# Kernel tuning notes

Measured on AMD Instinct MI355X. Metric: run time of the kernel, lower is better.

The kernel has to match this reference:

```python
import jax, jax.numpy as jnp
import numpy as np

D_MODEL = 2048
N_HEADS = 16
D_HEAD = D_MODEL // N_HEADS
ROPE_THETA = 10000.0


def setup_inputs() -> dict:
    key = jax.random.key(0)
    ks = jax.random.split(key, 3)
    B, T = 4, 2048
    x = jax.random.normal(ks[0], (B, T, D_MODEL), dtype=jnp.float32)
    # torch Linear weights stored transposed to (in, out) so y = x @ w + b
    w_qkv = jax.random.normal(ks[1], (D_MODEL, 3 * D_MODEL), dtype=jnp.float32) * (1.0 / np.sqrt(D_MODEL))
    b_qkv = jnp.zeros((3 * D_MODEL,), dtype=jnp.float32)
    w_out = jax.random.normal(ks[2], (D_MODEL, D_MODEL), dtype=jnp.float32) * (1.0 / np.sqrt(D_MODEL))
    b_out = jnp.zeros((D_MODEL,), dtype=jnp.float32)
    return {"x": x, "w_qkv": w_qkv, "b_qkv": b_qkv, "w_out": w_out, "b_out": b_out}


def _apply_rope(t, position_offset=0):
    # t: (B, H, T, d_head). Standard rotate-half RoPE.
    T = t.shape[2]
    inv_freq = 1.0 / (ROPE_THETA ** (jnp.arange(0, D_HEAD, 2, dtype=jnp.float32) / D_HEAD))
    pos = jnp.arange(T, dtype=jnp.float32) + position_offset
    freqs = jnp.einsum("t,f->tf", pos, inv_freq)            # (T, d_head/2)
    emb = jnp.concatenate([freqs, freqs], axis=-1)           # (T, d_head)
    cos = jnp.cos(emb)[None, None, :, :]
    sin = jnp.sin(emb)[None, None, :, :]
    t1, t2 = jnp.split(t, 2, axis=-1)
    rot = jnp.concatenate([-t2, t1], axis=-1)
    return t * cos + rot * sin


def reference(x, w_qkv, b_qkv, w_out, b_out):
    B, T, D = x.shape
    scale = 1.0 / np.sqrt(D_HEAD)
    qkv = x @ w_qkv + b_qkv                                   # (B, T, 3D)
    q, k, v = jnp.split(qkv, 3, axis=-1)
    def to_heads(a):
        return a.reshape(B, T, N_HEADS, D_HEAD).transpose(0, 2, 1, 3)  # (B,H,T,dh)
    q, k, v = to_heads(q), to_heads(k), to_heads(v)
    q = _apply_rope(q)
    k = _apply_rope(k)
    scores = jnp.einsum("bhqd,bhkd->bhqk", q, k) * scale      # (B,H,T,T)
    causal = jnp.triu(jnp.full((T, T), -jnp.inf, dtype=scores.dtype), k=1)
    scores = scores + causal
    attn = jax.nn.softmax(scores, axis=-1)                    # dropout p=0 (eval)
    ctx = jnp.einsum("bhqk,bhkd->bhqd", attn, v)
    ctx = ctx.transpose(0, 2, 1, 3).reshape(B, T, D)
    out = ctx @ w_out + b_out
    return out
```

## Files before the change

kernel.cpp:

```cpp
#include <hip/hip_runtime.h>

#define D_MODEL 2048
#define NHEADS 16
#define DHEAD 128
#define TSEQ 2048
#define BATCH 4
#define MROWS (BATCH*TSEQ)
#define NQKV (3*D_MODEL)
#define BH (BATCH*NHEADS)

typedef __attribute__((ext_vector_type(4))) float f32x4;
typedef __attribute__((ext_vector_type(8))) __bf16 bf16x8;
typedef __attribute__((ext_vector_type(4))) unsigned int u32x4;

__device__ inline unsigned short f2bf(float f) {
  union { float f; unsigned u; } v; v.f = f;
  unsigned r = (v.u + 0x7fffu + ((v.u >> 16) & 1u)) >> 16;
  return (unsigned short)r;
}
__device__ inline float bf2f(unsigned short h) {
  union { unsigned u; float f; } v; v.u = ((unsigned)h) << 16; return v.f;
}

__device__ inline void gl_lds16(const unsigned short* g, unsigned short* l) {
  __builtin_amdgcn_global_load_lds(
      (const __attribute__((address_space(1))) unsigned int*)g,
      (__attribute__((address_space(3))) unsigned int*)l, 16, 0, 0);
}

#define CFENCE asm volatile("" ::: "memory")
#define BAR do { CFENCE; __builtin_amdgcn_s_barrier(); CFENCE; } while (0)
#define VM(n) asm volatile("s_waitcnt vmcnt(" #n ")" ::: "memory")
#define LGKM0 asm volatile("s_waitcnt lgkmcnt(0)" ::: "memory")

__global__ __launch_bounds__(256) void cvt_bf16(const float* __restrict__ in,
                                                unsigned short* __restrict__ out, int n) {
  int i = (blockIdx.x * 256 + threadIdx.x) * 8;
  if (i >= n) return;
  float4 a = *(const float4*)(in + i);
  float4 b = *(const float4*)(in + i + 4);
  union { unsigned short s[8]; u32x4 v; } r;
  r.s[0] = f2bf(a.x); r.s[1] = f2bf(a.y); r.s[2] = f2bf(a.z); r.s[3] = f2bf(a.w);
  r.s[4] = f2bf(b.x); r.s[5] = f2bf(b.y); r.s[6] = f2bf(b.z); r.s[7] = f2bf(b.w);
  *(u32x4*)(out + i) = r.v;
}

__global__ __launch_bounds__(256) void transw(const float* __restrict__ w,
                                              unsigned short* __restrict__ wt, int K, int N) {
  __shared__ float tile[32][33];
  int n0 = blockIdx.x * 32, k0 = blockIdx.y * 32;
  int x = threadIdx.x & 31, y = threadIdx.x >> 5;
  #pragma unroll
  for (int j = 0; j < 4; ++j)
    tile[y + j * 8][x] = w[(size_t)(k0 + y + j * 8) * N + n0 + x];
  __syncthreads();
  #pragma unroll
  for (int j = 0; j < 4; ++j)
    wt[(size_t)(n0 + y + j * 8) * K + k0 + x] = f2bf(tile[x][y + j * 8]);
}

__global__ void rope_table(float2* __restrict__ tab) {
  int t = blockIdx.x, f = threadIdx.x;
  float inv = __expf(-0.14391156831212787f * (float)f);
  float ang = (float)t * inv;
  tab[t * 64 + f] = make_float2(cosf(ang), sinf(ang));
}

__global__ __launch_bounds__(256) void rope_apply(unsigned short* __restrict__ X,
                                                  const float2* __restrict__ tab,
                                                  float osc) {
  int row = blockIdx.x * 4 + (threadIdx.x >> 6);
  int f = threadIdx.x & 63;
  int t = row & (TSEQ - 1);
  unsigned short* p = X + (size_t)row * DHEAD;
  float2 cs = tab[t * 64 + f];
  float x1 = bf2f(p[f]), x2 = bf2f(p[f + 64]);
  p[f]      = f2bf((x1 * cs.x - x2 * cs.y) * osc);
  p[f + 64] = f2bf((x2 * cs.x + x1 * cs.y) * osc);
}

template<int MH, int NH>
__device__ inline void mmaq(f32x4 (&acc)[8][4], const bf16x8 (&av)[4][2], const bf16x8 (&bv)[2][2]) {
  #pragma unroll
  for (int m = 0; m < 4; ++m)
    #pragma unroll
    for (int n = 0; n < 2; ++n)
      #pragma unroll
      for (int kk = 0; kk < 2; ++kk)
        acc[MH * 4 + m][NH * 2 + n] =
            __builtin_amdgcn_mfma_f32_16x16x32_bf16(av[m][kk], bv[n][kk],
                                                    acc[MH * 4 + m][NH * 2 + n], 0, 0, 0);
}

__device__ inline void rdhalf(bf16x8 (&dst)[4][2], const unsigned short* base,
                              int rbase, int l15, int l16) {
  #pragma unroll
  for (int m = 0; m < 4; ++m)
    #pragma unroll
    for (int kk = 0; kk < 2; ++kk)
      dst[m][kk] = *(const bf16x8*)&base[(rbase + m * 16 + l15) * 64 +
                                         ((((kk << 2) | l16) ^ (l15 & 7)) << 3)];
}

__device__ inline void rdhalf2(bf16x8 (&dst)[2][2], const unsigned short* base,
                               int rbase, int l15, int l16) {
  #pragma unroll
  for (int n = 0; n < 2; ++n)
    #pragma unroll
    for (int kk = 0; kk < 2; ++kk)
      dst[n][kk] = *(const bf16x8*)&base[(rbase + n * 16 + l15) * 64 +
                                         ((((kk << 2) | l16) ^ (l15 & 7)) << 3)];
}

template<int MODE>
__global__ __launch_bounds__(512, 2) void gemm_bt(
    const unsigned short* __restrict__ A,
    const unsigned short* __restrict__ Bt,
    const float* __restrict__ bias,
    int M, int N, int K,
    unsigned short* __restrict__ Qb,
    unsigned short* __restrict__ Kb,
    unsigned short* __restrict__ VTb,
    float* __restrict__ outF)
{
  __shared__ unsigned short A_lds[2][2][128 * 64];
  __shared__ unsigned short B_lds[2][2][128 * 64];
  int tid = threadIdx.x;
  int wid = tid >> 6, lane = tid & 63;
  int wm = wid >> 2, wn = wid & 3;
  int l15 = lane & 15, l16 = lane >> 4;
  int row0 = blockIdx.y * 256, col0 = blockIdx.x * 256;

  const unsigned short* Ab = A + (size_t)row0 * K;
  const unsigned short* Bb = Bt + (size_t)col0 * K;
  int r8 = tid >> 3;
  int koff = (((tid & 7) ^ (r8 & 7)) << 3);

#define STAGE_A(par, h, tc) do { \
    const unsigned short* g_ = Ab + (size_t)((h) * 128 + r8) * K + (tc) + koff; \
    gl_lds16(g_, &A_lds[par][h][tid * 8]); \
    gl_lds16(g_ + (size_t)64 * K, &A_lds[par][h][(512 + tid) * 8]); } while (0)
#define STAGE_B(par, h, tc) do { \
    const unsigned short* g_ = Bb + (size_t)((h) * 128 + r8) * K + (tc) + koff; \
    gl_lds16(g_, &B_lds[par][h][tid * 8]); \
    gl_lds16(g_ + (size_t)64 * K, &B_lds[par][h][(512 + tid) * 8]); } while (0)

  f32x4 acc[8][4] = {};
  bf16x8 a0[4][2], a1[4][2], b0[2][2], b1[2][2];
  int NT = K >> 6;

  STAGE_A(0, 0, 0); STAGE_B(0, 0, 0); STAGE_A(0, 1, 0); STAGE_B(0, 1, 0);
  VM(4); BAR;

  for (int kt = 0; kt < NT - 1; ++kt) {
    int par = kt & 1, parn = par ^ 1;
    int kn = (kt + 1) << 6;
    rdhalf(a0, &A_lds[par][0][0], wm * 64, l15, l16);
    rdhalf2(b0, &B_lds[par][0][0], wn * 32, l15, l16);
    STAGE_A(parn, 0, kn); STAGE_B(parn, 0, kn);
    VM(6); BAR; LGKM0;
    __builtin_amdgcn_s_setprio(1);
    mmaq<0, 0>(acc, a0, b0);
    __builtin_amdgcn_s_setprio(0);
    rdhalf(a1, &A_lds[par][1][0], wm * 64, l15, l16);
    STAGE_A(parn, 1, kn);
    VM(6); BAR; LGKM0;
    __builtin_amdgcn_s_setprio(1);
    mmaq<1, 0>(acc, a1, b0);
    __builtin_amdgcn_s_setprio(0);
    rdhalf2(b1, &B_lds[par][1][0], wn * 32, l15, l16);
    STAGE_B(parn, 1, kn);
    __builtin_amdgcn_s_setprio(1);
    mmaq<0, 1>(acc, a0, b1);
    __builtin_amdgcn_s_setprio(0);
    VM(4); BAR;
    __builtin_amdgcn_s_setprio(1);
    mmaq<1, 1>(acc, a1, b1);
    __builtin_amdgcn_s_setprio(0);
  }

  {
    int par = (NT - 1) & 1;
    rdhalf(a0, &A_lds[par][0][0], wm * 64, l15, l16);
    rdhalf2(b0, &B_lds[par][0][0], wn * 32, l15, l16);
    VM(2); BAR; LGKM0;
    __builtin_amdgcn_s_setprio(1);
    mmaq<0, 0>(acc, a0, b0);
    __builtin_amdgcn_s_setprio(0);
    rdhalf(a1, &A_lds[par][1][0], wm * 64, l15, l16);
    VM(0); BAR;
    rdhalf2(b1, &B_lds[par][1][0], wn * 32, l15, l16);
    __builtin_amdgcn_s_setprio(1);
    mmaq<1, 0>(acc, a1, b0);
    mmaq<0, 1>(acc, a0, b1);
    mmaq<1, 1>(acc, a1, b1);
    __builtin_amdgcn_s_setprio(0);
  }

  #pragma unroll
  for (int am = 0; am < 8; ++am) {
    int mh = am >> 2, m = am & 3;
    #pragma unroll
    for (int an = 0; an < 4; ++an) {
      int nh = an >> 1, n = an & 1;
      int col = col0 + nh * 128 + wn * 32 + n * 16 + l15;
      float bs = bias[col];
      #pragma unroll
      for (int r = 0; r < 4; ++r) {
        int row = row0 + mh * 128 + wm * 64 + m * 16 + l16 * 4 + r;
        float val = acc[am][an][r] + bs;
        if (MODE == 0) {
          int which = col >> 11;
          int rem = col & 2047;
          int h = rem >> 7, dh = rem & 127;
          int b = row >> 11, t = row & 2047;
          int bh = b * NHEADS + h;
          if (which == 0)      Qb[((size_t)bh * TSEQ + t) * DHEAD + dh] = f2bf(val);
          else if (which == 1) Kb[((size_t)bh * TSEQ + t) * DHEAD + dh] = f2bf(val);
          else                 VTb[((size_t)bh * DHEAD + dh) * TSEQ + t] = f2bf(val);
        } else {
          outF[(size_t)row * N + col] = val;
        }
      }
    }
  }
#undef STAGE_A
#undef STAGE_B
}

__global__ __launch_bounds__(256, 2) void attn_fwd(
    const unsigned short* __restrict__ Qb,
    const unsigned short* __restrict__ Kb,
    const unsigned short* __restrict__ VTb,
    unsigned short* __restrict__ ctx)
{
  __shared__ unsigned short Ksm[2][64 * 128];
  __shared__ unsigned short Vsm[2][128 * 64];
  __shared__ unsigned short Psm[4][32 * 64];
  int bid = blockIdx.x;
  int bh = bid & 63, pr = bid >> 6;
  int hi = 15 - pr, lo = pr;
  int tid = threadIdx.x, wid = tid >> 6, lane = tid & 63;
  int l15 = lane & 15, l16 = lane >> 4;
  const unsigned short* Kh = Kb + (size_t)bh * TSEQ * DHEAD;
  const unsigned short* Vh = VTb + (size_t)bh * DHEAD * TSEQ;
  unsigned short* P = &Psm[wid][0];
  int swzl = (l15 & 7) << 4;

  int krow = tid >> 4;
  int kcol = (((tid & 15) << 4) ^ ((krow & 7) << 4)) >> 1;
  int vrow = tid >> 3;
  int vcol = (((tid & 7) << 4) ^ ((vrow & 7) << 4)) >> 1;
  int ldsl = tid * 8;

  int ck[4];
  #pragma unroll
  for (int kk = 0; kk < 4; ++kk) ck[kk] = ((kk * 64 + l16 * 16) ^ swzl) >> 1;

  bf16x8 qf[2][4];
  f32x4 accO[2][8];
  float mrow[2][4], lrow[2][4];

  int qbase = hi * 128 + wid * 32;
  #pragma unroll
  for (int m = 0; m < 2; ++m) {
    #pragma unroll
    for (int n = 0; n < 8; ++n) accO[m][n] = (f32x4)0.f;
    #pragma unroll
    for (int r = 0; r < 4; ++r) { mrow[m][r] = -1e30f; lrow[m][r] = 0.f; }
    #pragma unroll
    for (int kk = 0; kk < 4; ++kk)
      qf[m][kk] = *(const bf16x8*)&Qb[((size_t)bh * TSEQ + qbase + m * 16 + l15) * DHEAD
                                      + kk * 32 + l16 * 8];
  }

  int nt0 = 2 * hi + 2;
  int ntt = nt0 + 2 * lo + 2;

  {
    const unsigned short* kg = Kh + krow * DHEAD + kcol;
    const unsigned short* vg = Vh + (size_t)vrow * TSEQ + vcol;
    #pragma unroll
    for (int ps = 0; ps < 4; ++ps) {
      gl_lds16(kg + ps * 16 * DHEAD, &Ksm[0][ldsl + ps * 2048]);
      gl_lds16(vg + (size_t)ps * 32 * TSEQ, &Vsm[0][ldsl + ps * 2048]);
    }
  }
  __syncthreads();

  for (int it = 0; it < ntt; ++it) {
    int buf = it & 1;
    int kv0 = ((it >= nt0) ? (it - nt0) : it) * 64;

    if (it + 1 < ntt) {
      int n2 = it + 1;
      int kv2 = ((n2 >= nt0) ? (n2 - nt0) : n2) * 64;
      const unsigned short* kg = Kh + (size_t)(kv2 + krow) * DHEAD + kcol;
      const unsigned short* vg = Vh + (size_t)vrow * TSEQ + kv2 + vcol;
      #pragma unroll
      for (int ps = 0; ps < 4; ++ps) {
        gl_lds16(kg + ps * 16 * DHEAD, &Ksm[buf ^ 1][ldsl + ps * 2048]);
        gl_lds16(vg + (size_t)ps * 32 * TSEQ, &Vsm[buf ^ 1][ldsl + ps * 2048]);
      }
    }

    if (kv0 <= qbase + 31) {
      const unsigned short* Kt = Ksm[buf];
      const unsigned short* Vt = Vsm[buf];

      f32x4 S[2][4] = {};
      #pragma unroll
      for (int n = 0; n < 4; ++n) {
        bf16x8 kf[4];
        #pragma unroll
        for (int kk = 0; kk < 4; ++kk)
          kf[kk] = *(const bf16x8*)&Kt[(n * 16 + l15) * DHEAD + ck[kk]];
        #pragma unroll
        for (int m = 0; m < 2; ++m)
          #pragma unroll
          for (int kk = 0; kk < 4; ++kk)
            S[m][n] = __builtin_amdgcn_mfma_f32_16x16x32_bf16(qf[m][kk], kf[kk], S[m][n], 0, 0, 0);
      }

      bool masked = (kv0 + 63 > qbase);
      float vm_[2][4];
      float grow = -1e30f;
      #pragma unroll
      for (int m = 0; m < 2; ++m) {
        #pragma unroll
        for (int r = 0; r < 4; ++r) {
          if (masked) {
            int qg = qbase + m * 16 + l16 * 4 + r;
            if (kv0 + l15      > qg) S[m][0][r] = -1e30f;
            if (kv0 + 16 + l15 > qg) S[m][1][r] = -1e30f;
            if (kv0 + 32 + l15 > qg) S[m][2][r] = -1e30f;
            if (kv0 + 48 + l15 > qg) S[m][3][r] = -1e30f;
          }
          float v = fmaxf(fmaxf(S[m][0][r], S[m][1][r]), fmaxf(S[m][2][r], S[m][3][r]));
          #pragma unroll
          for (int off = 1; off < 16; off <<= 1) v = fmaxf(v, __shfl_xor(v, off));
          vm_[m][r] = v;
          grow = fmaxf(grow, v - mrow[m][r]);
        }
      }

      if (__any(grow > 8.f)) {
        #pragma unroll
        for (int m = 0; m < 2; ++m)
          #pragma unroll
          for (int r = 0; r < 4; ++r) {
            float mnew = fmaxf(mrow[m][r], vm_[m][r]);
            float alpha = exp2f(mrow[m][r] - mnew);
            mrow[m][r] = mnew;
            lrow[m][r] *= alpha;
            #pragma unroll
            for (int n = 0; n < 8; ++n) accO[m][n][r] *= alpha;
          }
      }

      #pragma unroll
      for (int m = 0; m < 2; ++m) {
        #pragma unroll
        for (int r = 0; r < 4; ++r) {
          float mr = mrow[m][r];
          float p0 = exp2f(S[m][0][r] - mr), p1 = exp2f(S[m][1][r] - mr);
          float p2 = exp2f(S[m][2][r] - mr), p3 = exp2f(S[m][3][r] - mr);
          float ps = (p0 + p1) + (p2 + p3);
          #pragma unroll
          for (int off = 1; off < 16; off <<= 1) ps += __shfl_xor(ps, off);
          lrow[m][r] += ps;
          int qr = m * 16 + l16 * 4 + r;
          int ws = (qr & 7) << 4;
          P[qr * 64 + ((((l15 << 1))      ^ ws) >> 1)] = f2bf(p0);
          P[qr * 64 + (((32 + (l15 << 1)) ^ ws) >> 1)] = f2bf(p1);
          P[qr * 64 + (((64 + (l15 << 1)) ^ ws) >> 1)] = f2bf(p2);
          P[qr * 64 + (((96 + (l15 << 1)) ^ ws) >> 1)] = f2bf(p3);
        }
      }

      bf16x8 pf[2][2];
      #pragma unroll
      for (int m = 0; m < 2; ++m)
        #pragma unroll
        for (int kk = 0; kk < 2; ++kk)
          pf[m][kk] = *(const bf16x8*)&P[(m * 16 + l15) * 64 + ck[kk]];
      #pragma unroll
      for (int n = 0; n < 8; ++n) {
        bf16x8 vf[2];
        #pragma unroll
        for (int kk = 0; kk < 2; ++kk)
          vf[kk] = *(const bf16x8*)&Vt[(n * 16 + l15) * 64 + ck[kk]];
        #pragma unroll
        for (int m = 0; m < 2; ++m)
          #pragma unroll
          for (int kk = 0; kk < 2; ++kk)
            accO[m][n] = __builtin_amdgcn_mfma_f32_16x16x32_bf16(pf[m][kk], vf[kk], accO[m][n], 0, 0, 0);
      }
    }

    if (it == nt0 - 1) {
      int b = bh >> 4, h = bh & 15;
      #pragma unroll
      for (int m = 0; m < 2; ++m)
        #pragma unroll
        for (int r = 0; r < 4; ++r) {
          float inv = 1.0f / lrow[m][r];
          int t = qbase + m * 16 + l16 * 4 + r;
          size_t base = ((size_t)b * TSEQ + t) * D_MODEL + h * DHEAD;
          #pragma unroll
          for (int n = 0; n < 8; ++n)
            ctx[base + n * 16 + l15] = f2bf(accO[m][n][r] * inv);
        }
      qbase = lo * 128 + wid * 32;
      #pragma unroll
      for (int m = 0; m < 2; ++m) {
        #pragma unroll
        for (int n = 0; n < 8; ++n) accO[m][n] = (f32x4)0.f;
        #pragma unroll
        for (int r = 0; r < 4; ++r) { mrow[m][r] = -1e30f; lrow[m][r] = 0.f; }
        #pragma unroll
        for (int kk = 0; kk < 4; ++kk)
          qf[m][kk] = *(const bf16x8*)&Qb[((size_t)bh * TSEQ + qbase + m * 16 + l15) * DHEAD
                                          + kk * 32 + l16 * 8];
      }
    }

    __syncthreads();
  }

  {
    int b = bh >> 4, h = bh & 15;
    #pragma unroll
    for (int m = 0; m < 2; ++m)
      #pragma unroll
      for (int r = 0; r < 4; ++r) {
        float inv = 1.0f / lrow[m][r];
        int t = qbase + m * 16 + l16 * 4 + r;
        size_t base = ((size_t)b * TSEQ + t) * D_MODEL + h * DHEAD;
        #pragma unroll
        for (int n = 0; n < 8; ++n)
          ctx[base + n * 16 + l15] = f2bf(accO[m][n][r] * inv);
      }
  }
}

extern "C" void kernel_launch(void* const* d_in, const int* in_sizes, int n_in,
                              void* d_out, int out_size, void* d_ws, size_t ws_size,
                              hipStream_t stream)
{
  const float* x     = (const float*)d_in[0];
  const float* w_qkv = (const float*)d_in[1];
  const float* b_qkv = (const float*)d_in[2];
  const float* w_out = (const float*)d_in[3];
  const float* b_out = (const float*)d_in[4];
  float* out = (float*)d_out;

  unsigned short* xb    = (unsigned short*)d_ws;
  unsigned short* wqkvT = xb    + (size_t)MROWS * D_MODEL;
  unsigned short* woutT = wqkvT + (size_t)NQKV * D_MODEL;
  unsigned short* Qb    = woutT + (size_t)D_MODEL * D_MODEL;
  unsigned short* Kb    = Qb    + (size_t)BH * TSEQ * DHEAD;
  unsigned short* VTb   = Kb    + (size_t)BH * TSEQ * DHEAD;
  float2* tab = (float2*)(VTb + (size_t)BH * TSEQ * DHEAD);

  const float SCALE_Q = 0.08838834764831845f * 1.4426950408889634f;

  cvt_bf16<<<MROWS * D_MODEL / 2048, 256, 0, stream>>>(x, xb, MROWS * D_MODEL);
  transw<<<dim3(NQKV / 32, D_MODEL / 32), 256, 0, stream>>>(w_qkv, wqkvT, D_MODEL, NQKV);
  transw<<<dim3(D_MODEL / 32, D_MODEL / 32), 256, 0, stream>>>(w_out, woutT, D_MODEL, D_MODEL);
  rope_table<<<TSEQ, 64, 0, stream>>>(tab);
  gemm_bt<0><<<dim3(NQKV / 256, MROWS / 256), 512, 0, stream>>>(
      xb, wqkvT, b_qkv, MROWS, NQKV, D_MODEL, Qb, Kb, VTb, nullptr);
  rope_apply<<<BH * TSEQ / 4, 256, 0, stream>>>(Qb, tab, SCALE_Q);
  rope_apply<<<BH * TSEQ / 4, 256, 0, stream>>>(Kb, tab, 1.0f);
  attn_fwd<<<dim3(512), 256, 0, stream>>>(Qb, Kb, VTb, xb);
  gemm_bt<1><<<dim3(D_MODEL / 256, MROWS / 256), 512, 0, stream>>>(
      xb, woutT, b_out, MROWS, D_MODEL, D_MODEL, nullptr, nullptr, nullptr, out);
}
```

Measured before the change: 514.0 us.

## Defer softmax row reductions in attention and truncate P to bf16

Each lane now keeps a local row max. The 16-lane shuffle max-reduction runs only inside the rare rescale branch. The per-tile shuffle sum of probabilities becomes per-lane partial sums, reduced once at the final normalisation. P is converted to bf16 by truncation instead of round-to-nearest-even. The aim is to remove many cross-lane shuffles and some ALU work from the inner KV loop, at the cost of slightly less accurate bf16 P values.

Result: faster. 466.6 us (-9.2%).

```diff
diff --git a/kernel.cpp b/kernel.cpp
--- a/kernel.cpp
+++ b/kernel.cpp
@@ -17,6 +17,10 @@
   union { float f; unsigned u; } v; v.f = f;
   unsigned r = (v.u + 0x7fffu + ((v.u >> 16) & 1u)) >> 16;
   return (unsigned short)r;
+}
+__device__ inline unsigned short f2bf_t(float f) {
+  union { float f; unsigned u; } v; v.f = f;
+  return (unsigned short)(v.u >> 16);
 }
 __device__ inline float bf2f(unsigned short h) {
   union { unsigned u; float f; } v; v.u = ((unsigned)h) << 16; return v.f;
@@ -323,7 +327,7 @@
       }
 
       bool masked = (kv0 + 63 > qbase);
-      float vm_[2][4];
+      float lmax[2][4];
       float grow = -1e30f;
       #pragma unroll
       for (int m = 0; m < 2; ++m) {
@@ -337,9 +341,7 @@
             if (kv0 + 48 + l15 > qg) S[m][3][r] = -1e30f;
           }
           float v = fmaxf(fmaxf(S[m][0][r], S[m][1][r]), fmaxf(S[m][2][r], S[m][3][r]));
-          #pragma unroll
-          for (int off = 1; off < 16; off <<= 1) v = fmaxf(v, __shfl_xor(v, off));
-          vm_[m][r] = v;
+          lmax[m][r] = v;
           grow = fmaxf(grow, v - mrow[m][r]);
         }
       }
@@ -349,7 +351,10 @@
         for (int m = 0; m < 2; ++m)
           #pragma unroll
           for (int r = 0; r < 4; ++r) {
-            float mnew = fmaxf(mrow[m][r], vm_[m][r]);
+            float v = lmax[m][r];
+            #pragma unroll
+            for (int off = 1; off < 16; off <<= 1) v = fmaxf(v, __shfl_xor(v, off));
+            float mnew = fmaxf(mrow[m][r], v);
             float alpha = exp2f(mrow[m][r] - mnew);
             mrow[m][r] = mnew;
             lrow[m][r] *= alpha;
@@ -365,16 +370,13 @@
           float mr = mrow[m][r];
           float p0 = exp2f(S[m][0][r] - mr), p1 = exp2f(S[m][1][r] - mr);
           float p2 = exp2f(S[m][2][r] - mr), p3 = exp2f(S[m][3][r] - mr);
-          float ps = (p0 + p1) + (p2 + p3);
-          #pragma unroll
-          for (int off = 1; off < 16; off <<= 1) ps += __shfl_xor(ps, off);
-          lrow[m][r] += ps;
+          lrow[m][r] += (p0 + p1) + (p2 + p3);
           int qr = m * 16 + l16 * 4 + r;
           int ws = (qr & 7) << 4;
-          P[qr * 64 + ((((l15 << 1))      ^ ws) >> 1)] = f2bf(p0);
-          P[qr * 64 + (((32 + (l15 << 1)) ^ ws) >> 1)] = f2bf(p1);
-          P[qr * 64 + (((64 + (l15 << 1)) ^ ws) >> 1)] = f2bf(p2);
-          P[qr * 64 + (((96 + (l15 << 1)) ^ ws) >> 1)] = f2bf(p3);
+          P[qr * 64 + ((((l15 << 1))      ^ ws) >> 1)] = f2bf_t(p0);
+          P[qr * 64 + (((32 + (l15 << 1)) ^ ws) >> 1)] = f2bf_t(p1);
+          P[qr * 64 + (((64 + (l15 << 1)) ^ ws) >> 1)] = f2bf_t(p2);
+          P[qr * 64 + (((96 + (l15 << 1)) ^ ws) >> 1)] = f2bf_t(p3);
         }
       }
 
@@ -404,7 +406,10 @@
       for (int m = 0; m < 2; ++m)
         #pragma unroll
         for (int r = 0; r < 4; ++r) {
-          float inv = 1.0f / lrow[m][r];
+          float ls = lrow[m][r];
+          #pragma unroll
+          for (int off = 1; off < 16; off <<= 1) ls += __shfl_xor(ls, off);
+          float inv = 1.0f / ls;
           int t = qbase + m * 16 + l16 * 4 + r;
           size_t base = ((size_t)b * TSEQ + t) * D_MODEL + h * DHEAD;
           #pragma unroll
@@ -434,7 +439,10 @@
     for (int m = 0; m < 2; ++m)
       #pragma unroll
       for (int r = 0; r < 4; ++r) {
-        float inv = 1.0f / lrow[m][r];
+        float ls = lrow[m][r];
+        #pragma unroll
+        for (int off = 1; off < 16; off <<= 1) ls += __shfl_xor(ls, off);
+        float inv = 1.0f / ls;
         int t = qbase + m * 16 + l16 * 4 + r;
         size_t base = ((size_t)b * TSEQ + t) * D_MODEL + h * DHEAD;
         #pragma unroll
```
